# Performance work log

Hardware: AMD Instinct MI355X
Metric: run time of the kernel (lower is better)

The kernel has to match this reference:

```python
import jax, jax.numpy as jnp
import numpy as np
import math

B, T, C = 4, 2048, 1024
H = 16
D = C // H  # head_dim = 64

def setup_inputs() -> dict:
    key = jax.random.key(0)
    k1, k2, k3 = jax.random.split(key, 3)
    x = jax.random.normal(k1, (B, T, C), dtype=jnp.float32)
    # weights stored as [in, out]; torch Linear weight is [out,in], applied as x @ W^T
    w_qkv = jax.random.normal(k2, (C, 3 * C), dtype=jnp.float32) * (1.0 / math.sqrt(C))
    w_proj = jax.random.normal(k3, (C, C), dtype=jnp.float32) * (1.0 / math.sqrt(C))
    return {"x": x, "w_qkv": w_qkv, "w_proj": w_proj}

def reference(x, w_qkv, w_proj):
    qkv = x @ w_qkv                                   # [B,T,3C]
    q, k, v = jnp.split(qkv, 3, axis=-1)
    # [B,T,C] -> [B,H,T,D]
    q = q.reshape(B, T, H, D).transpose(0, 2, 1, 3)
    k = k.reshape(B, T, H, D).transpose(0, 2, 1, 3)
    v = v.reshape(B, T, H, D).transpose(0, 2, 1, 3)
    scale = 1.0 / math.sqrt(D)
    att = jnp.einsum('bhqd,bhkd->bhqk', q, k) * scale  # [B,H,T,T]
    causal = jnp.tril(jnp.ones((T, T), dtype=bool))
    att = jnp.where(causal[None, None, :, :], att, jnp.float32(-jnp.inf))
    att = jax.nn.softmax(att, axis=-1)
    y = jnp.einsum('bhqk,bhkd->bhqd', att, v)          # [B,H,T,D]
    y = y.transpose(0, 2, 1, 3).reshape(B, T, C)
    return y @ w_proj
```

## Files before the change

kernel.cpp:

```cpp
#include <hip/hip_runtime.h>
#include <hip/hip_bf16.h>
#include <stdint.h>

typedef __attribute__((ext_vector_type(4))) float f32x4;
typedef __attribute__((ext_vector_type(8))) short bf16x8;
typedef __attribute__((ext_vector_type(2))) unsigned uint2v;

constexpr int BATCH = 4;
constexpr int SEQ   = 2048;
constexpr int CDIM  = 1024;
constexpr int NH    = 16;
constexpr int DH    = 64;
constexpr int MROWS = BATCH * SEQ;

__device__ __forceinline__ unsigned short f2bf(float f) {
  unsigned int u = __float_as_uint(f);
  u += 0x7FFFu + ((u >> 16) & 1u);
  return (unsigned short)(u >> 16);
}

__device__ __forceinline__ void gload16(const void* g, void* l) {
  __builtin_amdgcn_global_load_lds(
      (const __attribute__((address_space(1))) void*)g,
      (__attribute__((address_space(3))) void*)l, 16, 0, 0);
}

__device__ __forceinline__ unsigned cvtpk_bf16(float lo, float hi) {
  unsigned r;
  asm("v_cvt_pk_bf16_f32 %0, %1, %2" : "=v"(r) : "v"(lo), "v"(hi));
  return r;
}
__device__ __forceinline__ float crossmax4(float v) {
  uint2v r = __builtin_amdgcn_permlane32_swap(__float_as_uint(v), __float_as_uint(v), false, false);
  float m = fmaxf(__uint_as_float(r[0]), __uint_as_float(r[1]));
  uint2v r2 = __builtin_amdgcn_permlane16_swap(__float_as_uint(m), __float_as_uint(m), false, false);
  return fmaxf(__uint_as_float(r2[0]), __uint_as_float(r2[1]));
}
__device__ __forceinline__ float crosssum4(float v) {
  uint2v r = __builtin_amdgcn_permlane32_swap(__float_as_uint(v), __float_as_uint(v), false, false);
  float m = __uint_as_float(r[0]) + __uint_as_float(r[1]);
  uint2v r2 = __builtin_amdgcn_permlane16_swap(__float_as_uint(m), __float_as_uint(m), false, false);
  return __uint_as_float(r2[0]) + __uint_as_float(r2[1]);
}

__global__ __launch_bounds__(256) void k_cvt(const float* __restrict__ in,
                                             unsigned short* __restrict__ out, int n4) {
  int i = blockIdx.x * blockDim.x + threadIdx.x;
  int stride = gridDim.x * blockDim.x;
  for (; i < n4; i += stride) {
    float4 v = reinterpret_cast<const float4*>(in)[i];
    ushort4 o;
    o.x = f2bf(v.x); o.y = f2bf(v.y); o.z = f2bf(v.z); o.w = f2bf(v.w);
    reinterpret_cast<ushort4*>(out)[i] = o;
  }
}

__global__ __launch_bounds__(256) void k_tcvt(const float* __restrict__ in,
                                              unsigned short* __restrict__ out, int K, int N) {
  __shared__ float tile[32][33];
  int n0 = blockIdx.x * 32, k0 = blockIdx.y * 32;
  int tx = threadIdx.x, ty = threadIdx.y;
#pragma unroll
  for (int r = 0; r < 32; r += 8)
    tile[ty + r][tx] = in[(size_t)(k0 + ty + r) * N + n0 + tx];
  __syncthreads();
#pragma unroll
  for (int r = 0; r < 32; r += 8)
    out[(size_t)(n0 + ty + r) * K + k0 + tx] = f2bf(tile[tx][ty + r]);
}

template <int EPI>
__global__ __launch_bounds__(256) void k_gemm_bt(const unsigned short* __restrict__ A,
                                                 const unsigned short* __restrict__ Bt,
                                                 int M, int N, int K,
                                                 unsigned short* __restrict__ outQ,
                                                 unsigned short* __restrict__ outK,
                                                 unsigned short* __restrict__ outVt,
                                                 float* __restrict__ outC) {
  constexpr int BM = 128, BN = 128, BK = 64;
  __shared__ __align__(16) unsigned short smem[BM * BK * 2];
  unsigned short* As = smem;
  unsigned short* Bs = smem + BM * BK;
  const int nbn = N / BN;
  const int cpx = (nbn * (M / BM)) >> 3;
  const int orig = blockIdx.x;
  const int work = (orig & 7) * cpx + (orig >> 3);
  const int bn = work % nbn, bm = work / nbn;
  const int tid = threadIdx.x;
  const int lane = tid & 63, wave = tid >> 6;
  const int wm = wave >> 1, wn = wave & 1;
  const int l15 = lane & 15, l4 = lane >> 4;

  f32x4 acc[4][4];
#pragma unroll
  for (int i = 0; i < 4; ++i)
#pragma unroll
    for (int j = 0; j < 4; ++j) acc[i][j] = f32x4{0.f, 0.f, 0.f, 0.f};

  const int grow = lane >> 3;
  const int chL  = lane & 7;
  const int nk = K / BK;

  for (int kt = 0; kt < nk; ++kt) {
    __syncthreads();
#pragma unroll
    for (int c = 0; c < 4; ++c) {
      int row = wave * 32 + c * 8 + grow;
      int cg = chL ^ (row & 7);
      gload16(A + (size_t)(bm * BM + row) * K + kt * BK + cg * 8,
              reinterpret_cast<char*>(As) + (wave * 32 + c * 8) * 128);
      gload16(Bt + (size_t)(bn * BN + row) * K + kt * BK + cg * 8,
              reinterpret_cast<char*>(Bs) + (wave * 32 + c * 8) * 128);
    }
    asm volatile("s_waitcnt vmcnt(0)" ::: "memory");
    __syncthreads();
#pragma unroll
    for (int s = 0; s < 2; ++s) {
      bf16x8 af[4], bfr[4];
#pragma unroll
      for (int i = 0; i < 4; ++i) {
        int row = wm * 64 + i * 16 + l15;
        int off = row * 128 + ((s * 64 + l4 * 16) ^ ((row & 7) << 4));
        af[i] = *reinterpret_cast<const bf16x8*>(reinterpret_cast<char*>(As) + off);
      }
#pragma unroll
      for (int j = 0; j < 4; ++j) {
        int row = wn * 64 + j * 16 + l15;
        int off = row * 128 + ((s * 64 + l4 * 16) ^ ((row & 7) << 4));
        bfr[j] = *reinterpret_cast<const bf16x8*>(reinterpret_cast<char*>(Bs) + off);
      }
      __builtin_amdgcn_s_setprio(1);
#pragma unroll
      for (int i = 0; i < 4; ++i)
#pragma unroll
        for (int j = 0; j < 4; ++j)
          acc[i][j] = __builtin_amdgcn_mfma_f32_16x16x32_bf16(af[i], bfr[j], acc[i][j], 0, 0, 0);
      __builtin_amdgcn_s_setprio(0);
    }
  }

  if (EPI == 0) {
    const int sel = (bn * BN) >> 10;
    const float qsc = (sel == 0) ? 0.18033688f : 1.0f;
    char* stg = reinterpret_cast<char*>(smem);
    __syncthreads();
    const int b = (bm * BM) >> 11, tbase = (bm * BM) & 2047;
    if (sel < 2) {
#pragma unroll
      for (int i = 0; i < 4; ++i) {
        int wr = wm * 64 + i * 16 + l4 * 4;
#pragma unroll
        for (int j = 0; j < 4; ++j) {
          int wc = wn * 64 + j * 16 + l15;
#pragma unroll
          for (int r = 0; r < 4; ++r) {
            int row = wr + r;
            int off = row * 256 + ((wc * 2) ^ (((row >> 2) & 7) << 4));
            *reinterpret_cast<unsigned short*>(stg + off) = f2bf(acc[i][j][r] * qsc);
          }
        }
      }
      __syncthreads();
      unsigned short* dst = (sel == 0) ? outQ : outK;
#pragma unroll
      for (int ii = 0; ii < 8; ++ii) {
        int chunk = ii * 256 + tid;
        int row = chunk >> 4, ch = chunk & 15;
        int off = row * 256 + ((ch * 16) ^ (((row >> 2) & 7) << 4));
        uint4 ld = *reinterpret_cast<const uint4*>(stg + off);
        int n = bn * BN + ch * 8;
        int c = n & 1023, h = c >> 6, d = c & 63;
        *reinterpret_cast<uint4*>(dst + ((size_t)(b * NH + h) * SEQ + tbase + row) * DH + d) = ld;
      }
    } else {
#pragma unroll
      for (int i = 0; i < 4; ++i) {
        int wr = wm * 64 + i * 16 + l4 * 4;
#pragma unroll
        for (int j = 0; j < 4; ++j) {
          int wc = wn * 64 + j * 16 + l15;
          ushort4 pw;
          pw.x = f2bf(acc[i][j][0]); pw.y = f2bf(acc[i][j][1]);
          pw.z = f2bf(acc[i][j][2]); pw.w = f2bf(acc[i][j][3]);
          int off = wc * 256 + ((wr * 2) ^ ((wc & 7) << 4));
          *reinterpret_cast<ushort4*>(stg + off) = pw;
        }
      }
      __syncthreads();
#pragma unroll
      for (int ii = 0; ii < 8; ++ii) {
        int chunk = ii * 256 + tid;
        int col = chunk >> 4, tch = chunk & 15;
        int off = col * 256 + ((tch * 16) ^ ((col & 7) << 4));
        uint4 ld = *reinterpret_cast<const uint4*>(stg + off);
        int n = bn * BN + col;
        int c = n & 1023, h = c >> 6, d = c & 63;
        *reinterpret_cast<uint4*>(outVt + ((size_t)(b * NH + h) * DH + d) * SEQ + tbase + tch * 8) = ld;
      }
    }
  } else {
#pragma unroll
    for (int i = 0; i < 4; ++i) {
      int mbase = bm * BM + wm * 64 + i * 16 + l4 * 4;
#pragma unroll
      for (int j = 0; j < 4; ++j) {
        int n = bn * BN + wn * 64 + j * 16 + l15;
#pragma unroll
        for (int r = 0; r < 4; ++r)
          outC[(size_t)(mbase + r) * N + n] = acc[i][j][r];
      }
    }
  }
}

template <bool MASK>
__device__ __forceinline__ void attn_step(const unsigned short* __restrict__ Ksb,
                                          const unsigned short* __restrict__ Vsb,
                                          const bf16x8 (&qf)[2], f32x4 (&oacc)[4],
                                          float& mrun, float& lrun,
                                          int kb, int q, int l15, int l4) {
  f32x4 sac[4];
#pragma unroll
  for (int mf = 0; mf < 4; ++mf) {
    sac[mf] = f32x4{0.f, 0.f, 0.f, 0.f};
#pragma unroll
    for (int s = 0; s < 2; ++s) {
      int row = mf * 16 + l15;
      int off = row * 128 + ((s * 64 + l4 * 16) ^ ((row & 7) << 4));
      bf16x8 kf = *reinterpret_cast<const bf16x8*>(reinterpret_cast<const char*>(Ksb) + off);
      __builtin_amdgcn_s_setprio(1);
      sac[mf] = __builtin_amdgcn_mfma_f32_16x16x32_bf16(kf, qf[s], sac[mf], 0, 0, 0);
      __builtin_amdgcn_s_setprio(0);
    }
  }
  float tm = -1e30f;
#pragma unroll
  for (int mf = 0; mf < 4; ++mf)
#pragma unroll
    for (int r = 0; r < 4; ++r) {
      float x = sac[mf][r];
      if (MASK) {
        int key = kb + mf * 16 + l4 * 4 + r;
        if (key > q) x = -1e30f;
      }
      sac[mf][r] = x;
      tm = fmaxf(tm, x);
    }
  tm = crossmax4(tm);
  if (__any(tm > mrun + 8.f)) {
    float mnew = fmaxf(mrun, tm);
    float corr = __builtin_amdgcn_exp2f(mrun - mnew);
    lrun *= corr;
#pragma unroll
    for (int mf = 0; mf < 4; ++mf) {
      oacc[mf][0] *= corr; oacc[mf][1] *= corr;
      oacc[mf][2] *= corr; oacc[mf][3] *= corr;
    }
    mrun = mnew;
  }
  float ts = 0.f;
#pragma unroll
  for (int mf = 0; mf < 4; ++mf)
#pragma unroll
    for (int r = 0; r < 4; ++r) {
      float e = __builtin_amdgcn_exp2f(sac[mf][r] - mrun);
      sac[mf][r] = e;
      ts += e;
    }
  lrun += crosssum4(ts);
  bf16x8 pf[2];
#pragma unroll
  for (int s = 0; s < 2; ++s) {
    unsigned a0 = cvtpk_bf16(sac[2 * s][0], sac[2 * s][1]);
    unsigned a1 = cvtpk_bf16(sac[2 * s][2], sac[2 * s][3]);
    unsigned b0 = cvtpk_bf16(sac[2 * s + 1][0], sac[2 * s + 1][1]);
    unsigned b1 = cvtpk_bf16(sac[2 * s + 1][2], sac[2 * s + 1][3]);
    uint2v r0 = __builtin_amdgcn_permlane32_swap(a0, b0, false, false);
    uint2v r1 = __builtin_amdgcn_permlane32_swap(a1, b1, false, false);
    uint2v q0 = __builtin_amdgcn_permlane16_swap(r0[0], r0[1], false, false);
    uint2v q1 = __builtin_amdgcn_permlane16_swap(r1[0], r1[1], false, false);
    union { unsigned u[4]; bf16x8 v; } t;
    t.u[0] = q0[0]; t.u[1] = q1[0]; t.u[2] = q0[1]; t.u[3] = q1[1];
    pf[s] = t.v;
  }
#pragma unroll
  for (int mf = 0; mf < 4; ++mf) {
#pragma unroll
    for (int s = 0; s < 2; ++s) {
      int row = mf * 16 + l15;
      int off = row * 128 + ((s * 64 + l4 * 16) ^ ((row & 7) << 4));
      bf16x8 vf = *reinterpret_cast<const bf16x8*>(reinterpret_cast<const char*>(Vsb) + off);
      __builtin_amdgcn_s_setprio(1);
      oacc[mf] = __builtin_amdgcn_mfma_f32_16x16x32_bf16(vf, pf[s], oacc[mf], 0, 0, 0);
      __builtin_amdgcn_s_setprio(0);
    }
  }
}

__global__ __launch_bounds__(512, 8) void k_attn(const unsigned short* __restrict__ Qg,
                                                 const unsigned short* __restrict__ Kg,
                                                 const unsigned short* __restrict__ Vtg,
                                                 unsigned short* __restrict__ Yg) {
  __shared__ __align__(16) unsigned short Ks[2][64 * 64];
  __shared__ __align__(16) unsigned short Vs[2][64 * 64];

  const int orig = blockIdx.x;
  const int work = (orig & 7) * 128 + (orig >> 3);
  const int jb = work & 15;
  const int bh = work >> 4;
  const int h = bh & (NH - 1), b = bh >> 4;
  const int tid = threadIdx.x;
  const int lane = tid & 63, wave = tid >> 6;
  const int l15 = lane & 15, l4 = lane >> 4;
  const int wgrp = wave >> 2, wsub = wave & 3;

  const int qtB = 31 - jb;
  const int myqt = wgrp ? jb : qtB;
  const int q = myqt * 64 + wsub * 16 + l15;

  bf16x8 qf[2];
#pragma unroll
  for (int s = 0; s < 2; ++s)
    qf[s] = *reinterpret_cast<const bf16x8*>(Qg + ((size_t)bh * SEQ + q) * DH + s * 32 + l4 * 8);

  f32x4 oacc[4];
#pragma unroll
  for (int mf = 0; mf < 4; ++mf) oacc[mf] = f32x4{0.f, 0.f, 0.f, 0.f};
  float mrun = -1e30f, lrun = 0.f;

  const int srow = wave * 8 + (lane >> 3);
  const int scg  = (lane & 7) ^ (srow & 7);
  const size_t kbg = (size_t)bh * SEQ * DH;
  const size_t vbg = (size_t)bh * DH * SEQ;

  gload16(Kg + kbg + (size_t)srow * DH + scg * 8,
          reinterpret_cast<char*>(&Ks[0][0]) + wave * 1024);
  gload16(Vtg + vbg + (size_t)srow * SEQ + scg * 8,
          reinterpret_cast<char*>(&Vs[0][0]) + wave * 1024);
  asm volatile("s_waitcnt vmcnt(0)" ::: "memory");
  __syncthreads();

  int cur = 0;
  for (int kt = 0; kt <= qtB; ++kt) {
    const int kb = kt * 64;
    if (kt < qtB) {
      const int kb2 = kb + 64;
      gload16(Kg + kbg + (size_t)(kb2 + srow) * DH + scg * 8,
              reinterpret_cast<char*>(&Ks[cur ^ 1][0]) + wave * 1024);
      gload16(Vtg + vbg + (size_t)srow * SEQ + kb2 + scg * 8,
              reinterpret_cast<char*>(&Vs[cur ^ 1][0]) + wave * 1024);
    }
    if (kt <= myqt) {
      if (kt == myqt) attn_step<true>(&Ks[cur][0], &Vs[cur][0], qf, oacc, mrun, lrun, kb, q, l15, l4);
      else            attn_step<false>(&Ks[cur][0], &Vs[cur][0], qf, oacc, mrun, lrun, kb, q, l15, l4);
    }
    asm volatile("s_waitcnt vmcnt(0)" ::: "memory");
    __syncthreads();
    cur ^= 1;
  }

  const float inv = 1.f / lrun;
  char* stg = reinterpret_cast<char*>(&Ks[0][0]) + wave * 2048;
#pragma unroll
  for (int mf = 0; mf < 4; ++mf) {
    ushort4 ov;
    ov.x = f2bf(oacc[mf][0] * inv); ov.y = f2bf(oacc[mf][1] * inv);
    ov.z = f2bf(oacc[mf][2] * inv); ov.w = f2bf(oacc[mf][3] * inv);
    int off = l15 * 128 + ((mf * 32 + l4 * 8) ^ ((l15 & 7) << 4));
    *reinterpret_cast<ushort4*>(stg + off) = ov;
  }
  const int qbase = myqt * 64 + wsub * 16;
#pragma unroll
  for (int ii = 0; ii < 2; ++ii) {
    int c = ii * 64 + lane;
    int row = c >> 3, ch = c & 7;
    int off = row * 128 + ((ch * 16) ^ ((row & 7) << 4));
    uint4 ld = *reinterpret_cast<const uint4*>(stg + off);
    *reinterpret_cast<uint4*>(Yg + (size_t)(b * SEQ + qbase + row) * CDIM + h * 64 + ch * 8) = ld;
  }
}

extern "C" void kernel_launch(void* const* d_in, const int* in_sizes, int n_in,
                              void* d_out, int out_size, void* d_ws, size_t ws_size,
                              hipStream_t stream) {
  const float* x      = (const float*)d_in[0];
  const float* w_qkv  = (const float*)d_in[1];
  const float* w_proj = (const float*)d_in[2];
  float* out = (float*)d_out;
  char* ws = (char*)d_ws;

  unsigned short* Xb  = (unsigned short*)(ws);
  unsigned short* WqT = (unsigned short*)(ws + (size_t)16777216);
  unsigned short* WpT = (unsigned short*)(ws + (size_t)23068672);
  unsigned short* Q   = (unsigned short*)(ws + (size_t)25165824);
  unsigned short* K   = (unsigned short*)(ws + (size_t)41943040);
  unsigned short* Vt  = (unsigned short*)(ws + (size_t)58720256);
  unsigned short* Y   = Xb;

  k_cvt<<<2048, 256, 0, stream>>>(x, Xb, (BATCH * SEQ * CDIM) / 4);
  k_tcvt<<<dim3((3 * CDIM) / 32, CDIM / 32), dim3(32, 8), 0, stream>>>(w_qkv, WqT, CDIM, 3 * CDIM);
  k_tcvt<<<dim3(CDIM / 32, CDIM / 32), dim3(32, 8), 0, stream>>>(w_proj, WpT, CDIM, CDIM);

  k_gemm_bt<0><<<1536, 256, 0, stream>>>(
      Xb, WqT, MROWS, 3 * CDIM, CDIM, Q, K, Vt, nullptr);

  k_attn<<<1024, 512, 0, stream>>>(Q, K, Vt, Y);

  k_gemm_bt<1><<<512, 256, 0, stream>>>(
      Y, WpT, MROWS, CDIM, CDIM, nullptr, nullptr, nullptr, out);
}
```

Measured before the change: 173.5 us.

## Software-pipeline attention: compute next tile's QK^T while current tile does softmax-PV

Splits the per-tile attention step into a QK^T stage and a softmax+PV stage. The QK^T for the next K tile is issued right after the current tile's softmax and PV work. K is now prefetched two tiles ahead and V one tile ahead, with double-buffered LDS slots reused so the S scores for the next tile are ready when the loop iterates. It also widens the s_setprio regions to cover whole MFMA loops instead of toggling around each instruction. The aim is to overlap the exp/max/shuffle work with matrix-core work and cut per-MFMA priority toggles, at the cost of extra live registers for the carried scores and a prologue load and sync.

```diff
diff --git a/kernel.cpp b/kernel.cpp
--- a/kernel.cpp
+++ b/kernel.cpp
@@ -213,13 +213,10 @@
   }
 }
 
-template <bool MASK>
-__device__ __forceinline__ void attn_step(const unsigned short* __restrict__ Ksb,
-                                          const unsigned short* __restrict__ Vsb,
-                                          const bf16x8 (&qf)[2], f32x4 (&oacc)[4],
-                                          float& mrun, float& lrun,
-                                          int kb, int q, int l15, int l4) {
-  f32x4 sac[4];
+__device__ __forceinline__ void qkt8(const unsigned short* __restrict__ Ksb,
+                                     const bf16x8 (&qf)[2], f32x4 (&sac)[4],
+                                     int l15, int l4) {
+  __builtin_amdgcn_s_setprio(1);
 #pragma unroll
   for (int mf = 0; mf < 4; ++mf) {
     sac[mf] = f32x4{0.f, 0.f, 0.f, 0.f};
@@ -228,11 +225,17 @@
       int row = mf * 16 + l15;
       int off = row * 128 + ((s * 64 + l4 * 16) ^ ((row & 7) << 4));
       bf16x8 kf = *reinterpret_cast<const bf16x8*>(reinterpret_cast<const char*>(Ksb) + off);
-      __builtin_amdgcn_s_setprio(1);
       sac[mf] = __builtin_amdgcn_mfma_f32_16x16x32_bf16(kf, qf[s], sac[mf], 0, 0, 0);
-      __builtin_amdgcn_s_setprio(0);
-    }
-  }
+    }
+  }
+  __builtin_amdgcn_s_setprio(0);
+}
+
+template <bool MASK>
+__device__ __forceinline__ void smpv(const unsigned short* __restrict__ Vsb,
+                                     f32x4 (&sac)[4], f32x4 (&oacc)[4],
+                                     float& mrun, float& lrun,
+                                     int kb, int q, int l15, int l4) {
   float tm = -1e30f;
 #pragma unroll
   for (int mf = 0; mf < 4; ++mf)
@@ -283,6 +286,7 @@
     t.u[0] = q0[0]; t.u[1] = q1[0]; t.u[2] = q0[1]; t.u[3] = q1[1];
     pf[s] = t.v;
   }
+  __builtin_amdgcn_s_setprio(1);
 #pragma unroll
   for (int mf = 0; mf < 4; ++mf) {
 #pragma unroll
@@ -290,11 +294,10 @@
       int row = mf * 16 + l15;
       int off = row * 128 + ((s * 64 + l4 * 16) ^ ((row & 7) << 4));
       bf16x8 vf = *reinterpret_cast<const bf16x8*>(reinterpret_cast<const char*>(Vsb) + off);
-      __builtin_amdgcn_s_setprio(1);
       oacc[mf] = __builtin_amdgcn_mfma_f32_16x16x32_bf16(vf, pf[s], oacc[mf], 0, 0, 0);
-      __builtin_amdgcn_s_setprio(0);
-    }
-  }
+    }
+  }
+  __builtin_amdgcn_s_setprio(0);
 }
 
 __global__ __launch_bounds__(512, 8) void k_attn(const unsigned short* __restrict__ Qg,
@@ -337,26 +340,30 @@
           reinterpret_cast<char*>(&Ks[0][0]) + wave * 1024);
   gload16(Vtg + vbg + (size_t)srow * SEQ + scg * 8,
           reinterpret_cast<char*>(&Vs[0][0]) + wave * 1024);
+  gload16(Kg + kbg + (size_t)(64 + srow) * DH + scg * 8,
+          reinterpret_cast<char*>(&Ks[1][0]) + wave * 1024);
   asm volatile("s_waitcnt vmcnt(0)" ::: "memory");
   __syncthreads();
 
-  int cur = 0;
+  f32x4 sac[4];
+  qkt8(&Ks[0][0], qf, sac, l15, l4);
+  __syncthreads();
+
   for (int kt = 0; kt <= qtB; ++kt) {
-    const int kb = kt * 64;
-    if (kt < qtB) {
-      const int kb2 = kb + 64;
-      gload16(Kg + kbg + (size_t)(kb2 + srow) * DH + scg * 8,
-              reinterpret_cast<char*>(&Ks[cur ^ 1][0]) + wave * 1024);
-      gload16(Vtg + vbg + (size_t)srow * SEQ + kb2 + scg * 8,
-              reinterpret_cast<char*>(&Vs[cur ^ 1][0]) + wave * 1024);
-    }
+    if (kt + 2 <= qtB)
+      gload16(Kg + kbg + (size_t)((kt + 2) * 64 + srow) * DH + scg * 8,
+              reinterpret_cast<char*>(&Ks[kt & 1][0]) + wave * 1024);
+    if (kt + 1 <= qtB)
+      gload16(Vtg + vbg + (size_t)srow * SEQ + (kt + 1) * 64 + scg * 8,
+              reinterpret_cast<char*>(&Vs[(kt + 1) & 1][0]) + wave * 1024);
     if (kt <= myqt) {
-      if (kt == myqt) attn_step<true>(&Ks[cur][0], &Vs[cur][0], qf, oacc, mrun, lrun, kb, q, l15, l4);
-      else            attn_step<false>(&Ks[cur][0], &Vs[cur][0], qf, oacc, mrun, lrun, kb, q, l15, l4);
-    }
+      if (kt == myqt) smpv<true>(&Vs[kt & 1][0], sac, oacc, mrun, lrun, kt * 64, q, l15, l4);
+      else            smpv<false>(&Vs[kt & 1][0], sac, oacc, mrun, lrun, kt * 64, q, l15, l4);
+    }
+    if (kt + 1 <= myqt)
+      qkt8(&Ks[(kt + 1) & 1][0], qf, sac, l15, l4);
     asm volatile("s_waitcnt vmcnt(0)" ::: "memory");
     __syncthreads();
-    cur ^= 1;
   }
 
   const float inv = 1.f / lrun;
```

Result: slower. 183.8 us (+6.0%).

## Triple-buffer K tiles with two-ahead prefetch and partial vmcnt waits

Applied to the files above, without the earlier changes.

Changes the attention loop's K staging from double to triple buffering, so K is prefetched two tiles ahead and V one tile ahead. The end-of-iteration wait becomes vmcnt(1) instead of vmcnt(0), leaving the next-next K load in flight across the barrier, and __syncthreads is replaced by sched_barrier plus s_barrier. The aim is to hide more global-load latency behind the MFMA work. It costs an extra 8 KB of LDS per block, which could lower occupancy, and it depends on the load completion order matching the vmcnt accounting.

```diff
diff --git a/kernel.cpp b/kernel.cpp
--- a/kernel.cpp
+++ b/kernel.cpp
@@ -301,8 +301,8 @@
                                                  const unsigned short* __restrict__ Kg,
                                                  const unsigned short* __restrict__ Vtg,
                                                  unsigned short* __restrict__ Yg) {
-  __shared__ __align__(16) unsigned short Ks[2][64 * 64];
-  __shared__ __align__(16) unsigned short Vs[2][64 * 64];
+  __shared__ __align__(16) unsigned short K3[3][64 * 64];
+  __shared__ __align__(16) unsigned short V2[2][64 * 64];
 
   const int orig = blockIdx.x;
   const int work = (orig & 7) * 128 + (orig >> 3);
@@ -334,33 +334,39 @@
   const size_t vbg = (size_t)bh * DH * SEQ;
 
   gload16(Kg + kbg + (size_t)srow * DH + scg * 8,
-          reinterpret_cast<char*>(&Ks[0][0]) + wave * 1024);
+          reinterpret_cast<char*>(&K3[0][0]) + wave * 1024);
+  gload16(Kg + kbg + (size_t)(64 + srow) * DH + scg * 8,
+          reinterpret_cast<char*>(&K3[1][0]) + wave * 1024);
   gload16(Vtg + vbg + (size_t)srow * SEQ + scg * 8,
-          reinterpret_cast<char*>(&Vs[0][0]) + wave * 1024);
+          reinterpret_cast<char*>(&V2[0][0]) + wave * 1024);
   asm volatile("s_waitcnt vmcnt(0)" ::: "memory");
   __syncthreads();
 
-  int cur = 0;
+  int kcur = 0;
+  int k2dst = 2;
   for (int kt = 0; kt <= qtB; ++kt) {
-    const int kb = kt * 64;
-    if (kt < qtB) {
-      const int kb2 = kb + 64;
-      gload16(Kg + kbg + (size_t)(kb2 + srow) * DH + scg * 8,
-              reinterpret_cast<char*>(&Ks[cur ^ 1][0]) + wave * 1024);
-      gload16(Vtg + vbg + (size_t)srow * SEQ + kb2 + scg * 8,
-              reinterpret_cast<char*>(&Vs[cur ^ 1][0]) + wave * 1024);
-    }
+    if (kt + 1 <= qtB)
+      gload16(Vtg + vbg + (size_t)srow * SEQ + (kt + 1) * 64 + scg * 8,
+              reinterpret_cast<char*>(&V2[(kt + 1) & 1][0]) + wave * 1024);
+    if (kt + 2 <= qtB)
+      gload16(Kg + kbg + (size_t)((kt + 2) * 64 + srow) * DH + scg * 8,
+              reinterpret_cast<char*>(&K3[k2dst][0]) + wave * 1024);
     if (kt <= myqt) {
-      if (kt == myqt) attn_step<true>(&Ks[cur][0], &Vs[cur][0], qf, oacc, mrun, lrun, kb, q, l15, l4);
-      else            attn_step<false>(&Ks[cur][0], &Vs[cur][0], qf, oacc, mrun, lrun, kb, q, l15, l4);
-    }
-    asm volatile("s_waitcnt vmcnt(0)" ::: "memory");
-    __syncthreads();
-    cur ^= 1;
+      const unsigned short* Kc = &K3[kcur][0];
+      const unsigned short* Vc = &V2[kt & 1][0];
+      if (kt == myqt) attn_step<true>(Kc, Vc, qf, oacc, mrun, lrun, kt * 64, q, l15, l4);
+      else            attn_step<false>(Kc, Vc, qf, oacc, mrun, lrun, kt * 64, q, l15, l4);
+    }
+    if (kt + 2 <= qtB) asm volatile("s_waitcnt vmcnt(1)" ::: "memory");
+    else               asm volatile("s_waitcnt vmcnt(0)" ::: "memory");
+    __builtin_amdgcn_sched_barrier(0);
+    __builtin_amdgcn_s_barrier();
+    kcur = (kcur == 2) ? 0 : kcur + 1;
+    k2dst = (k2dst == 2) ? 0 : k2dst + 1;
   }
 
   const float inv = 1.f / lrun;
-  char* stg = reinterpret_cast<char*>(&Ks[0][0]) + wave * 2048;
+  char* stg = reinterpret_cast<char*>(&K3[0][0]) + wave * 2048;
 #pragma unroll
   for (int mf = 0; mf < 4; ++mf) {
     ushort4 ov;
```

New measurement: 160.5 us. 1.08x faster.
